# Optimization experiments

Hardware: AMD Instinct MI355X
Metric: run time of the kernel (lower is better)

The kernel has to match this reference:

```python
import jax, jax.numpy as jnp
import numpy as np

NH = 50000; NO = 50000; E = 500000; D = 256; L = 8; B = 512; C = 117


def setup_inputs() -> dict:
    key = jax.random.key(0)
    ks = jax.random.split(key, 32)
    s = 0.05
    inp = {
        'x_human': jax.random.normal(ks[0], (NH, D), jnp.float32),
        'x_object': jax.random.normal(ks[1], (NO, D), jnp.float32),
        'edge_index_ho': jax.random.randint(ks[2], (2, E), 0, NH),
        'edge_index_oh': jax.random.randint(ks[3], (2, E), 0, NO),
        'edge_attr_ho': jax.random.normal(ks[4], (E, 2), jnp.float32),
        'edge_attr_oh': jax.random.normal(ks[5], (E, 2), jnp.float32),
        'hbatch': jnp.sort(jax.random.randint(ks[6], (NH,), 0, B)),
        'obatch': jnp.sort(jax.random.randint(ks[7], (NO,), 0, B)),
    }
    # GATConv params per relation, stacked over L layers
    names = ['Wsrc', 'Wdst', 'asrc', 'adst', 'Wedge', 'aedge', 'bias']
    shapes = [(L, D, D), (L, D, D), (L, D), (L, D), (L, 2, D), (L, D), (L, D)]
    i = 8
    for rel in ['ho', 'oh']:
        for n, sh in zip(names, shapes):
            inp[f'{n}_{rel}'] = jax.random.normal(ks[i], sh, jnp.float32) * s
            i += 1
    inp['W_emlp'] = jax.random.normal(ks[i], (2, 32), jnp.float32) * s
    inp['b_emlp'] = jnp.zeros((32,), jnp.float32)
    inp['W_p1'] = jax.random.normal(ks[i + 1], (2 * D + 32, C), jnp.float32) * s
    inp['b_p1'] = jnp.zeros((C,), jnp.float32)
    inp['W_p2'] = jax.random.normal(ks[i + 2], (2 * D + 32, C), jnp.float32) * s
    inp['b_p2'] = jnp.zeros((C,), jnp.float32)
    return inp


def _gat(x_src, x_dst, ei, ea, Wsrc, Wdst, asrc, adst, Wedge, aedge, bias, num_dst):
    # PyG GATConv (heads=1, edge_dim=2, add_self_loops=False)
    h_src = x_src @ Wsrc                       # [Ns, D]
    h_dst = x_dst @ Wdst                       # [Nd, D]
    src, dst = ei[0], ei[1]
    a_s = h_src @ asrc                         # [Ns]
    a_d = h_dst @ adst                         # [Nd]
    a_e = (ea @ Wedge) @ aedge                 # [E]
    logit = jax.nn.leaky_relu(a_s[src] + a_d[dst] + a_e, 0.2)
    m = jax.ops.segment_max(logit, dst, num_segments=num_dst)
    ex = jnp.exp(logit - m[dst])
    denom = jax.ops.segment_sum(ex, dst, num_segments=num_dst)
    alpha = ex / denom[dst]                    # segment softmax over dst
    out = jax.ops.segment_sum(h_src[src] * alpha[:, None], dst, num_segments=num_dst)
    return out + bias


def _seg_mean(x, seg, num):
    s = jax.ops.segment_sum(x, seg, num_segments=num)
    cnt = jax.ops.segment_sum(jnp.ones((x.shape[0],), x.dtype), seg, num_segments=num)
    return s / jnp.maximum(cnt, 1.0)[:, None]


def reference(x_human, x_object, edge_index_ho, edge_index_oh, edge_attr_ho,
              edge_attr_oh, hbatch, obatch,
              Wsrc_ho, Wdst_ho, asrc_ho, adst_ho, Wedge_ho, aedge_ho, bias_ho,
              Wsrc_oh, Wdst_oh, asrc_oh, adst_oh, Wedge_oh, aedge_oh, bias_oh,
              W_emlp, b_emlp, W_p1, b_p1, W_p2, b_p2):
    xh, xo = x_human, x_object
    ph, po = None, None
    for l in range(L):
        nxo = _gat(xh, xo, edge_index_ho, edge_attr_ho, Wsrc_ho[l], Wdst_ho[l],
                   asrc_ho[l], adst_ho[l], Wedge_ho[l], aedge_ho[l], bias_ho[l], NO)
        nxh = _gat(xo, xh, edge_index_oh, edge_attr_oh, Wsrc_oh[l], Wdst_oh[l],
                   asrc_oh[l], adst_oh[l], Wedge_oh[l], aedge_oh[l], bias_oh[l], NH)
        nxh = jax.nn.relu(nxh)
        nxo = jax.nn.relu(nxo)
        if ph is not None:
            nxh = nxh + ph
            nxo = nxo + po
        ph, po = nxh, nxo
        xh, xo = nxh, nxo
    hpool = _seg_mean(xh, hbatch, B)           # [B, D]
    opool = _seg_mean(xo, obatch, B)           # [B, D]
    ea = jax.nn.relu(edge_attr_ho @ W_emlp + b_emlp)  # [E, 32]
    edge_batch = hbatch[edge_index_ho[0]]
    epool = _seg_mean(ea, edge_batch, B)       # [B, 32]
    graph_emb = jnp.concatenate([hpool, opool, epool], axis=-1)  # [B, 544]
    l1 = jax.nn.softmax(graph_emb @ W_p1 + b_p1, axis=1)
    l2 = jax.nn.softmax(graph_emb @ W_p2 + b_p2, axis=1)
    return jnp.stack((l1, l2), axis=1)         # [B, 2, C]
```

## Files before the change

### kernel.cpp

```cpp
#include <hip/hip_runtime.h>
#include <math.h>


#define NNODE 50000
#define EDG   500000
#define DIM   256
#define LAY   8
#define BB    512
#define CC    117
#define EMBD  544
#define SCB   49
#define HW    16384
#define HC    16
#define HNW   4

typedef short bf16x8 __attribute__((ext_vector_type(8)));
typedef float f32x4  __attribute__((ext_vector_type(4)));

static __device__ __forceinline__ float lrelu(float x){ return x >= 0.f ? x : 0.2f*x; }
static __device__ __forceinline__ unsigned short f2b(float f){
  unsigned int u = __float_as_uint(f);
  unsigned int r = (u + 0x7fffu + ((u >> 16) & 1u)) >> 16;
  return (unsigned short)r;
}
static __device__ __forceinline__ float b2f(unsigned short u){
  return __uint_as_float(((unsigned int)u) << 16);
}
static __device__ __forceinline__ float blo(unsigned int u){
  return __uint_as_float(u << 16);
}
static __device__ __forceinline__ float bhi(unsigned int u){
  return __uint_as_float(u & 0xffff0000u);
}
static __device__ __forceinline__ unsigned cvtpk(float lo, float hi){
  unsigned r;
  asm("v_cvt_pk_bf16_f32 %0, %1, %2" : "=v"(r) : "v"(lo), "v"(hi));
  return r;
}
static __device__ __forceinline__ float rdlane_f(float v, int id){
  return __uint_as_float(__builtin_amdgcn_readlane(__float_as_uint(v), id));
}
static __device__ __forceinline__ int rdlane_i(int v, int id){
  return __builtin_amdgcn_readlane(v, id);
}

static __device__ __forceinline__ void gload_lds16(const void* g, void* l){
  __builtin_amdgcn_global_load_lds((const __attribute__((address_space(1))) void*)g,
                                   (__attribute__((address_space(3))) void*)l,
                                   16, 0, 0);
}

__global__ void vcompute_k(const float* __restrict__ Wsho, const float* __restrict__ Wdho,
                           const float* __restrict__ asho, const float* __restrict__ adho,
                           const float* __restrict__ Wsoh, const float* __restrict__ Wdoh,
                           const float* __restrict__ asoh, const float* __restrict__ adoh,
                           float* __restrict__ vbuf){
  int gid = blockIdx.x*blockDim.x + threadIdx.x;
  int wv = gid >> 6, lane = gid & 63;
  if (wv >= 32*DIM) return;
  int p = wv >> 8, k = wv & 255;
  int which = p & 1, rel = (p>>1)&1, l = p>>2;
  const float* W; const float* a;
  if (rel==0){ W = which? Wdho : Wsho; a = which? adho : asho; }
  else       { W = which? Wdoh : Wsoh; a = which? adoh : asoh; }
  W += (size_t)l*DIM*DIM; a += (size_t)l*DIM;
  const float4* w4 = (const float4*)(W + (size_t)k*DIM);
  const float4* a4 = (const float4*)a;
  float4 wv4 = w4[lane], av4 = a4[lane];
  float s = wv4.x*av4.x + wv4.y*av4.y + wv4.z*av4.z + wv4.w*av4.w;
  for (int off=32; off; off>>=1) s += __shfl_xor(s, off);
  if (lane==0) vbuf[(size_t)p*DIM + k] = s;
}

__global__ void wecompute_k(const float* __restrict__ Weho, const float* __restrict__ aeho,
                            const float* __restrict__ Weoh, const float* __restrict__ aeoh,
                            float* __restrict__ webuf){
  int blk = blockIdx.x;
  int rel = blk & 1, l = blk >> 1;
  const float* We = rel? Weoh : Weho;
  const float* ae = rel? aeoh : aeho;
  int lane = threadIdx.x;
  const float4* w0 = (const float4*)(We + (size_t)l*2*DIM);
  const float4* w1 = (const float4*)(We + (size_t)l*2*DIM + DIM);
  const float4* a4 = (const float4*)(ae + (size_t)l*DIM);
  float4 av = a4[lane], x0 = w0[lane], x1 = w1[lane];
  float s0 = x0.x*av.x + x0.y*av.y + x0.z*av.z + x0.w*av.w;
  float s1 = x1.x*av.x + x1.y*av.y + x1.z*av.z + x1.w*av.w;
  for (int off=32; off; off>>=1){ s0 += __shfl_xor(s0, off); s1 += __shfl_xor(s1, off); }
  if (lane==0){ webuf[blk*2] = s0; webuf[blk*2+1] = s1; }
}

__global__ void histp_k(const int* __restrict__ ei_ho, const int* __restrict__ ei_oh,
                        int* __restrict__ phist){
  __shared__ int h[HW];
  int x = blockIdx.x, y = blockIdx.y, z = blockIdx.z, t = threadIdx.x;
  for (int i=t; i<HW; i+=256) h[i] = 0;
  __syncthreads();
  const int* keys = (z==0)? (ei_ho + EDG) : (z==1)? (ei_oh + EDG) : ei_ho;
  int lo = y << 14;
  int e0 = x * (EDG/HC), e1 = e0 + (EDG/HC);
  for (int e = e0 + t; e < e1; e += 256){
    int k = keys[e] - lo;
    if ((unsigned)k < (unsigned)HW) atomicAdd(&h[k], 1);
  }
  __syncthreads();
  int* dst = phist + (size_t)(((z*HNW + y)*HC + x))*HW;
  for (int i=t; i<HW; i+=256) dst[i] = h[i];
}

static __device__ __forceinline__ int4 phist_sum4(const int* __restrict__ phist,
                                                  int z, int idx){
  int win = idx >> 14, off = idx & (HW-1);
  const int* base = phist + (size_t)((z*HNW + win)*HC)*HW + off;
  int4 s = make_int4(0,0,0,0);
  #pragma unroll
  for (int c=0;c<HC;c++){
    int4 v = *(const int4*)(base + (size_t)c*HW);
    s.x += v.x; s.y += v.y; s.z += v.z; s.w += v.w;
  }
  return s;
}

__global__ void scanA_k(const int* __restrict__ phist, int* __restrict__ bsum){
  __shared__ int sh[256];
  int y = blockIdx.y, b = blockIdx.x, t = threadIdx.x;
  int idx = b*1024 + t*4;
  int s = 0;
  if (idx + 3 < NNODE){
    int4 v = phist_sum4(phist, y, idx);
    s = v.x + v.y + v.z + v.w;
  } else {
    for (int j=0;j<4;j++) if (idx+j < NNODE){
      int win = (idx+j) >> 14, off = (idx+j) & (HW-1);
      for (int c=0;c<HC;c++) s += phist[(size_t)((y*HNW+win)*HC+c)*HW + off];
    }
  }
  sh[t] = s; __syncthreads();
  for (int off=128; off; off>>=1){ if (t<off) sh[t] += sh[t+off]; __syncthreads(); }
  if (t==0) bsum[y*SCB + b] = sh[0];
}

__global__ void scanB_k(int* __restrict__ bsum, int* __restrict__ boff,
                        int* __restrict__ rp0, int* __restrict__ rp1, int* __restrict__ rp2){
  int t = threadIdx.x;
  if (t >= 3) return;
  int run = 0;
  for (int i=0;i<SCB;i++){ boff[t*SCB+i] = run; run += bsum[t*SCB+i]; }
  int* rp = (t==0)? rp0 : (t==1)? rp1 : rp2;
  rp[NNODE] = run;
}

__global__ void scanC_k(const int* __restrict__ phist, const int* __restrict__ boff,
                        int* __restrict__ rp0, int* __restrict__ rp1, int* __restrict__ rp2){
  __shared__ int sh[256];
  int y = blockIdx.y, b = blockIdx.x, t = threadIdx.x;
  int* rp = (y==0)? rp0 : (y==1)? rp1 : rp2;
  int idx = b*1024 + t*4;
  int c[4] = {0,0,0,0};
  if (idx + 3 < NNODE){
    int4 v = phist_sum4(phist, y, idx);
    c[0]=v.x; c[1]=v.y; c[2]=v.z; c[3]=v.w;
  } else {
    for (int j=0;j<4;j++) if (idx+j < NNODE){
      int win = (idx+j) >> 14, off = (idx+j) & (HW-1);
      for (int cc=0;cc<HC;cc++) c[j] += phist[(size_t)((y*HNW+win)*HC+cc)*HW + off];
    }
  }
  int mysum = c[0]+c[1]+c[2]+c[3];
  sh[t] = mysum; __syncthreads();
  for (int off=1; off<256; off<<=1){
    int v = (t>=off) ? sh[t-off] : 0;
    __syncthreads();
    sh[t] += v;
    __syncthreads();
  }
  int base = boff[y*SCB + b] + (sh[t] - mysum);
  int run = 0;
  for (int j=0;j<4;j++){
    if (idx+j < NNODE) rp[idx+j] = base + run;
    run += c[j];
  }
}

__global__ void scatter3_k(const int* __restrict__ ei_ho, const int* __restrict__ ei_oh,
                           const float* __restrict__ ea_ho, const float* __restrict__ ea_oh,
                           const int* __restrict__ rp0, const int* __restrict__ rp1,
                           const int* __restrict__ rp2, int* __restrict__ cur,
                           float4* __restrict__ rec0, float4* __restrict__ rec1,
                           float2* __restrict__ eap2){
  int e = blockIdx.x*blockDim.x + threadIdx.x;
  if (e >= EDG) return;
  int y = blockIdx.y;
  if (y == 0){
    int d = ei_ho[EDG + e];
    int pos = rp0[d] + atomicAdd(&cur[d], 1);
    rec0[pos] = make_float4(__int_as_float(ei_ho[e]), ea_ho[2*e], ea_ho[2*e+1], 0.f);
  } else if (y == 1){
    int d = ei_oh[EDG + e];
    int pos = rp1[d] + atomicAdd(&cur[NNODE + d], 1);
    rec1[pos] = make_float4(__int_as_float(ei_oh[e]), ea_oh[2*e], ea_oh[2*e+1], 0.f);
  } else {
    int s = ei_ho[e];
    int pos = rp2[s] + atomicAdd(&cur[2*NNODE + s], 1);
    eap2[pos] = make_float2(ea_ho[2*e], ea_ho[2*e+1]);
  }
}

__global__ void xcdg_k(const float* __restrict__ xh_in, const float* __restrict__ xo_in,
                       unsigned short* __restrict__ xhb, unsigned short* __restrict__ xob,
                       const float* __restrict__ vbuf, float* __restrict__ aset){
  int gid = blockIdx.x*blockDim.x + threadIdx.x;
  int w = gid >> 6, lane = gid & 63;
  if (w >= NNODE) return;
  int z = blockIdx.y;
  const float* X = z? xo_in : xh_in;
  unsigned short* O = z? xob : xhb;
  const float* v1 = vbuf + (size_t)(z? 2:0)*DIM;
  const float* v2 = vbuf + (size_t)(z? 1:3)*DIM;
  float* o1 = aset + (size_t)(z? 2:0)*NNODE;
  float* o2 = aset + (size_t)(z? 1:3)*NNODE;
  float4 xv = ((const float4*)(X + (size_t)w*DIM))[lane];
  uint2 ob; ob.x = cvtpk(xv.x, xv.y); ob.y = cvtpk(xv.z, xv.w);
  ((uint2*)O)[(size_t)w*64 + lane] = ob;
  float4 a = ((const float4*)v1)[lane];
  float4 b = ((const float4*)v2)[lane];
  float s1 = xv.x*a.x + xv.y*a.y + xv.z*a.z + xv.w*a.w;
  float s2 = xv.x*b.x + xv.y*b.y + xv.z*b.z + xv.w*b.w;
  for (int off=32; off; off>>=1){ s1 += __shfl_xor(s1, off); s2 += __shfl_xor(s2, off); }
  if (lane==0){ o1[w] = s1; o2[w] = s2; }
}

__global__ void wtconv_k(const float* __restrict__ Who, const float* __restrict__ Woh,
                         unsigned short* __restrict__ Wt){
  int gid = blockIdx.x*blockDim.x + threadIdx.x;
  int rel = gid >> 19;
  int rem = gid & ((1<<19)-1);
  int l = rem >> 16;
  int idx = rem & 65535;
  int n = idx >> 8, k = idx & 255;
  const float* W = rel ? Woh : Who;
  Wt[gid] = f2b(W[(size_t)l*65536 + (size_t)k*256 + n]);
}

__global__ __launch_bounds__(256) void gemmb2_k(const unsigned short* __restrict__ A0,
                                                const unsigned short* __restrict__ A1,
                                                const unsigned short* __restrict__ B0,
                                                const unsigned short* __restrict__ B1,
                                                unsigned short* __restrict__ H0,
                                                unsigned short* __restrict__ H1, int M){
  __shared__ __align__(16) unsigned short As[4096];
  __shared__ __align__(16) unsigned short Bs[4096];
  int z = blockIdx.z;
  const unsigned short* A  = z? A1 : A0;
  const unsigned short* Bt = z? B1 : B0;
  unsigned short* H        = z? H1 : H0;
  int tid = threadIdx.x;
  int col0 = blockIdx.x * 128;
  int row0 = blockIdx.y * 128;
  int w = tid >> 6, lane = tid & 63;
  int q = lane >> 4, ml = lane & 15;
  f32x4 acc[2][8];
  #pragma unroll
  for (int i=0;i<2;i++)
    #pragma unroll
    for (int j=0;j<8;j++) acc[i][j] = (f32x4){0.f,0.f,0.f,0.f};

  const unsigned short* srcA[2];
  const unsigned short* srcB[2];
  #pragma unroll
  for (int p=0;p<2;p++){
    int c = p*256 + w*64 + lane;
    int row = ((c>>6)<<4) | (c&15);
    int sq  = (c>>4)&3;
    int gr = row0 + row; if (gr >= M) gr = M-1;
    srcA[p] = A  + (size_t)gr*256 + sq*8;
    srcB[p] = Bt + (size_t)(col0 + row)*256 + sq*8;
  }

  for (int k0 = 0; k0 < 256; k0 += 32){
    #pragma unroll
    for (int p = 0; p < 2; ++p){
      gload_lds16(srcA[p], &As[(size_t)(p*256 + w*64)*8]);
      gload_lds16(srcB[p], &Bs[(size_t)(p*256 + w*64)*8]);
      srcA[p] += 32; srcB[p] += 32;
    }
    __syncthreads();
    bf16x8 a0 = *(const bf16x8*)&As[(((2*w+0)*4 + q)*16 + ml)*8];
    bf16x8 a1 = *(const bf16x8*)&As[(((2*w+1)*4 + q)*16 + ml)*8];
    #pragma unroll
    for (int nf = 0; nf < 8; ++nf){
      bf16x8 b = *(const bf16x8*)&Bs[((nf*4 + q)*16 + ml)*8];
      acc[0][nf] = __builtin_amdgcn_mfma_f32_16x16x32_bf16(a0, b, acc[0][nf], 0,0,0);
      acc[1][nf] = __builtin_amdgcn_mfma_f32_16x16x32_bf16(a1, b, acc[1][nf], 0,0,0);
    }
    __syncthreads();
  }
  #pragma unroll
  for (int mf = 0; mf < 2; ++mf){
    #pragma unroll
    for (int r = 0; r < 4; ++r){
      int gr = row0 + 32*w + 16*mf + q*4 + r;
      if (gr < M){
        #pragma unroll
        for (int nf = 0; nf < 8; ++nf)
          H[(size_t)gr*256 + col0 + nf*16 + ml] = f2b(acc[mf][nf][r]);
      }
    }
  }
}

__global__ void attn2_k(const int* __restrict__ rp0, const float4* __restrict__ rec0,
                        const int* __restrict__ rp1, const float4* __restrict__ rec1,
                        const float* __restrict__ cur_a, float* __restrict__ nxt_a,
                        const float* __restrict__ wepl,
                        const unsigned short* __restrict__ hs0,
                        const unsigned short* __restrict__ hs1,
                        const float* __restrict__ bias0, const float* __restrict__ bias1,
                        const unsigned short* __restrict__ xprev0,
                        const unsigned short* __restrict__ xprev1,
                        unsigned short* __restrict__ xnext0,
                        unsigned short* __restrict__ xnext1,
                        const float* __restrict__ vbl,
                        int hasRes, int doNext){
  int gid = blockIdx.x*blockDim.x + threadIdx.x;
  int w = gid >> 6, lane = gid & 63;
  if (w >= NNODE) return;
  int rel = blockIdx.y;
  const int* rowptr = rel? rp1 : rp0;
  const float4* rec = rel? rec1 : rec0;
  const float* a_s = cur_a + (size_t)(rel? 2:0)*NNODE;
  const float* a_d = cur_a + (size_t)(rel? 3:1)*NNODE;
  float w0 = wepl[rel? 2:0], w1 = wepl[rel? 3:1];
  const unsigned short* hs = rel? hs1 : hs0;
  const float* bias = rel? bias1 : bias0;
  const unsigned short* xprev = rel? xprev1 : xprev0;
  unsigned short* xnext = rel? xnext1 : xnext0;

  int st = rowptr[w], en = rowptr[w+1];
  int deg = en - st;
  float adv = a_d[w];

  float4 bv = ((const float4*)bias)[lane];
  uint2 rres = ((const uint2*)xprev)[(size_t)w*64 + lane];
  float4 va = ((const float4*)(vbl + (size_t)(rel? 0:2)*DIM))[lane];
  float4 vc = ((const float4*)(vbl + (size_t)(rel? 3:1)*DIM))[lane];

  float ax=0.f, ay=0.f, az=0.f, aw=0.f;
  if (deg > 0 && deg <= 64){
    int sreg = 0; float lg = -INFINITY;
    if (lane < deg){
      float4 r = rec[st + lane];
      sreg = __float_as_int(r.x);
      lg = lrelu(a_s[sreg] + adv + r.y*w0 + r.z*w1);
    }
    float mx = lg;
    for (int off=32; off; off>>=1) mx = fmaxf(mx, __shfl_xor(mx, off));
    float ex = (lane < deg) ? __expf(lg - mx) : 0.f;
    float sm = ex;
    for (int off=32; off; off>>=1) sm += __shfl_xor(sm, off);
    float wgt = ex * __builtin_amdgcn_rcpf(sm);
    int i = 0;
    for (; i + 7 < deg; i += 8){
      float wi[8]; const uint2* rp[8];
      #pragma unroll
      for (int j=0;j<8;j++){
        wi[j] = rdlane_f(wgt, i+j);
        rp[j] = (const uint2*)(hs + (size_t)rdlane_i(sreg, i+j)*DIM);
      }
      uint2 hv[8];
      #pragma unroll
      for (int j=0;j<8;j++) hv[j] = rp[j][lane];
      #pragma unroll
      for (int j=0;j<8;j++){
        ax += wi[j]*blo(hv[j].x); ay += wi[j]*bhi(hv[j].x);
        az += wi[j]*blo(hv[j].y); aw += wi[j]*bhi(hv[j].y);
      }
    }
    for (; i + 3 < deg; i += 4){
      float wi[4]; const uint2* rp[4];
      #pragma unroll
      for (int j=0;j<4;j++){
        wi[j] = rdlane_f(wgt, i+j);
        rp[j] = (const uint2*)(hs + (size_t)rdlane_i(sreg, i+j)*DIM);
      }
      uint2 hv[4];
      #pragma unroll
      for (int j=0;j<4;j++) hv[j] = rp[j][lane];
      #pragma unroll
      for (int j=0;j<4;j++){
        ax += wi[j]*blo(hv[j].x); ay += wi[j]*bhi(hv[j].x);
        az += wi[j]*blo(hv[j].y); aw += wi[j]*bhi(hv[j].y);
      }
    }
    for (; i < deg; ++i){
      float wi = rdlane_f(wgt, i);
      const uint2* rp = (const uint2*)(hs + (size_t)rdlane_i(sreg, i)*DIM);
      uint2 hv = rp[lane];
      ax += wi*blo(hv.x); ay += wi*bhi(hv.x);
      az += wi*blo(hv.y); aw += wi*bhi(hv.y);
    }
  } else if (deg > 64){
    const ushort4* h4 = (const ushort4*)hs;
    float mx = -INFINITY;
    for (int p = st + lane; p < en; p += 64){
      float4 r = rec[p];
      float lg = lrelu(a_s[__float_as_int(r.x)] + adv + r.y*w0 + r.z*w1);
      mx = fmaxf(mx, lg);
    }
    for (int off=32; off; off>>=1) mx = fmaxf(mx, __shfl_xor(mx, off));
    float sm = 0.f;
    for (int p = st + lane; p < en; p += 64){
      float4 r = rec[p];
      float lg = lrelu(a_s[__float_as_int(r.x)] + adv + r.y*w0 + r.z*w1);
      sm += __expf(lg - mx);
    }
    for (int off=32; off; off>>=1) sm += __shfl_xor(sm, off);
    float inv = __builtin_amdgcn_rcpf(sm);
    for (int p = st; p < en; ++p){
      float4 r = rec[p];
      int s = __float_as_int(r.x);
      float lg = lrelu(a_s[s] + adv + r.y*w0 + r.z*w1);
      float wgt = __expf(lg - mx) * inv;
      ushort4 hv = h4[(size_t)s*64 + lane];
      ax += wgt*b2f(hv.x); ay += wgt*b2f(hv.y); az += wgt*b2f(hv.z); aw += wgt*b2f(hv.w);
    }
  }

  float resw = hasRes ? 1.f : 0.f;
  float4 o;
  o.x = fmaxf(ax + bv.x, 0.f) + resw*blo(rres.x);
  o.y = fmaxf(ay + bv.y, 0.f) + resw*bhi(rres.x);
  o.z = fmaxf(az + bv.z, 0.f) + resw*blo(rres.y);
  o.w = fmaxf(aw + bv.w, 0.f) + resw*bhi(rres.y);
  uint2 ob; ob.x = cvtpk(o.x, o.y); ob.y = cvtpk(o.z, o.w);
  ((uint2*)xnext)[(size_t)w*64 + lane] = ob;
  if (doNext){
    float s1 = o.x*va.x + o.y*va.y + o.z*va.z + o.w*va.w;
    float s2 = o.x*vc.x + o.y*vc.y + o.z*vc.z + o.w*vc.w;
    for (int off=32; off; off>>=1){ s1 += __shfl_xor(s1, off); s2 += __shfl_xor(s2, off); }
    if (lane==0){
      float* asn = nxt_a + (size_t)(rel? 0:2)*NNODE;
      float* adn = nxt_a + (size_t)(rel? 3:1)*NNODE;
      asn[w] = s1; adn[w] = s2;
    }
  }
}

__device__ __forceinline__ int lowerb(const int* a, int n, int v){
  int lo=0, hi=n;
  while (lo < hi){ int m = (lo+hi)>>1; if (a[m] < v) lo = m+1; else hi = m; }
  return lo;
}

__global__ void pool2_k(const unsigned short* __restrict__ xh, const unsigned short* __restrict__ xo,
                        const int* __restrict__ hbatch, const int* __restrict__ obatch,
                        float* __restrict__ hpool, float* __restrict__ opool){
  int z = blockIdx.y;
  const unsigned short* x = z? xo : xh;
  const int* batch = z? obatch : hbatch;
  float* out = z? opool : hpool;
  int b = blockIdx.x, t = threadIdx.x;
  int st = lowerb(batch, NNODE, b), en = lowerb(batch, NNODE, b+1);
  float s = 0.f;
  for (int i=st;i<en;i++) s += b2f(x[(size_t)i*DIM + t]);
  out[(size_t)b*DIM + t] = s / fmaxf((float)(en - st), 1.f);
}

__global__ void epool_k(const int* __restrict__ rp_src, const int* __restrict__ hbatch,
                        const float2* __restrict__ eaperm, const float* __restrict__ Wem,
                        const float* __restrict__ bem, float* __restrict__ epool){
  __shared__ float ps[8][33];
  int b = blockIdx.x, t = threadIdx.x;
  int j = t & 31, g = t >> 5;
  int nst = lowerb(hbatch, NNODE, b), nen = lowerb(hbatch, NNODE, b+1);
  int est = rp_src[nst], een = rp_src[nen];
  float w0 = Wem[j], w1 = Wem[32+j], bb = bem[j];
  float s = 0.f;
  for (int p = est + g; p < een; p += 8){
    float2 e = eaperm[p];
    s += fmaxf(e.x*w0 + e.y*w1 + bb, 0.f);
  }
  ps[g][j] = s; __syncthreads();
  if (g == 0){
    float tot = 0.f;
    #pragma unroll
    for (int gg=0; gg<8; gg++) tot += ps[gg][j];
    epool[(size_t)b*32 + j] = tot / fmaxf((float)(een - est), 1.f);
  }
}

__global__ void head_k(const float* __restrict__ hpool, const float* __restrict__ opool,
                       const float* __restrict__ epool,
                       const float* __restrict__ Wp1, const float* __restrict__ bp1,
                       const float* __restrict__ Wp2, const float* __restrict__ bp2,
                       float* __restrict__ out){
  __shared__ float emb[EMBD];
  __shared__ float red[256];
  int b = blockIdx.x, t = threadIdx.x;
  emb[t] = hpool[(size_t)b*DIM + t];
  emb[DIM + t] = opool[(size_t)b*DIM + t];
  if (t < 32) emb[2*DIM + t] = epool[(size_t)b*32 + t];
  __syncthreads();
  for (int h = 0; h < 2; ++h){
    const float* Wp = h? Wp2 : Wp1;
    const float* bp = h? bp2 : bp1;
    float logit = -INFINITY;
    if (t < CC){
      float s = bp[t];
      for (int k=0;k<EMBD;k++) s += emb[k]*Wp[(size_t)k*CC + t];
      logit = s;
    }
    red[t] = logit; __syncthreads();
    for (int off=128; off; off>>=1){ if (t<off) red[t] = fmaxf(red[t], red[t+off]); __syncthreads(); }
    float mx = red[0]; __syncthreads();
    float ex = (t < CC) ? expf(logit - mx) : 0.f;
    red[t] = ex; __syncthreads();
    for (int off=128; off; off>>=1){ if (t<off) red[t] += red[t+off]; __syncthreads(); }
    float sm = red[0]; __syncthreads();
    if (t < CC) out[((size_t)b*2 + h)*CC + t] = ex / sm;
  }
}

extern "C" void kernel_launch(void* const* d_in, const int* in_sizes, int n_in,
                              void* d_out, int out_size, void* d_ws, size_t ws_size,
                              hipStream_t stream) {
  (void)in_sizes; (void)n_in; (void)out_size; (void)ws_size;
  const float* xh_in   = (const float*)d_in[0];
  const float* xo_in   = (const float*)d_in[1];
  const int*   ei_ho   = (const int*)d_in[2];
  const int*   ei_oh   = (const int*)d_in[3];
  const float* ea_ho   = (const float*)d_in[4];
  const float* ea_oh   = (const float*)d_in[5];
  const int*   hbatch  = (const int*)d_in[6];
  const int*   obatch  = (const int*)d_in[7];
  const float* Wsrc_ho = (const float*)d_in[8];
  const float* Wdst_ho = (const float*)d_in[9];
  const float* asrc_ho = (const float*)d_in[10];
  const float* adst_ho = (const float*)d_in[11];
  const float* Wedge_ho= (const float*)d_in[12];
  const float* aedge_ho= (const float*)d_in[13];
  const float* bias_ho = (const float*)d_in[14];
  const float* Wsrc_oh = (const float*)d_in[15];
  const float* Wdst_oh = (const float*)d_in[16];
  const float* asrc_oh = (const float*)d_in[17];
  const float* adst_oh = (const float*)d_in[18];
  const float* Wedge_oh= (const float*)d_in[19];
  const float* aedge_oh= (const float*)d_in[20];
  const float* bias_oh = (const float*)d_in[21];
  const float* W_emlp  = (const float*)d_in[22];
  const float* b_emlp  = (const float*)d_in[23];
  const float* W_p1    = (const float*)d_in[24];
  const float* b_p1    = (const float*)d_in[25];
  const float* W_p2    = (const float*)d_in[26];
  const float* b_p2    = (const float*)d_in[27];
  float* out = (float*)d_out;

  size_t ND = (size_t)NNODE*DIM;
  float* f = (float*)d_ws;
  float* aset0 = f;
  float* aset1 = aset0 + 4*NNODE;
  float* vbuf  = aset1 + 4*NNODE;
  float* webuf = vbuf + 32*DIM;
  float* hpool = webuf + 32;
  float* opool = hpool + (size_t)BB*DIM;
  float* epool = opool + (size_t)BB*DIM;
  float4* rec_ho  = (float4*)(epool + (size_t)BB*32);
  float4* rec_oh  = rec_ho + EDG;
  float2* eap_src = (float2*)(rec_oh + EDG);
  unsigned short* xhb0 = (unsigned short*)(eap_src + EDG);
  unsigned short* xhb1 = xhb0 + ND;
  unsigned short* xob0 = xhb1 + ND;
  unsigned short* xob1 = xob0 + ND;
  unsigned short* hSb0 = xob1 + ND;
  unsigned short* hSb1 = hSb0 + ND;
  unsigned short* Wtb  = hSb1 + ND;
  int* cur     = (int*)(Wtb + (size_t)2*LAY*DIM*DIM);
  int* rp_ho   = cur + 3*NNODE;
  int* rp_oh   = rp_ho + NNODE + 1;
  int* rp_src  = rp_oh + NNODE + 1;
  int* bsum    = rp_src + NNODE + 1;
  int* boff    = bsum + 3*SCB;
  int* phist   = boff + 3*SCB;

  hipMemsetAsync(cur, 0, sizeof(int)*3*NNODE, stream);
  vcompute_k<<<2048, 256, 0, stream>>>(Wsrc_ho, Wdst_ho, asrc_ho, adst_ho,
                                       Wsrc_oh, Wdst_oh, asrc_oh, adst_oh, vbuf);
  wecompute_k<<<16, 64, 0, stream>>>(Wedge_ho, aedge_ho, Wedge_oh, aedge_oh, webuf);
  wtconv_k<<<4096, 256, 0, stream>>>(Wsrc_ho, Wsrc_oh, Wtb);
  histp_k<<<dim3(HC, HNW, 3), 256, 0, stream>>>(ei_ho, ei_oh, phist);
  scanA_k<<<dim3(SCB, 3), 256, 0, stream>>>(phist, bsum);
  scanB_k<<<1, 64, 0, stream>>>(bsum, boff, rp_ho, rp_oh, rp_src);
  scanC_k<<<dim3(SCB, 3), 256, 0, stream>>>(phist, boff, rp_ho, rp_oh, rp_src);
  scatter3_k<<<dim3(1954, 3), 256, 0, stream>>>(ei_ho, ei_oh, ea_ho, ea_oh,
                                                rp_ho, rp_oh, rp_src, cur,
                                                rec_ho, rec_oh, eap_src);
  xcdg_k<<<dim3(12500, 2), 256, 0, stream>>>(xh_in, xo_in, xhb1, xob1, vbuf, aset0);

  const unsigned short* xh = xhb1;
  const unsigned short* xo = xob1;
  unsigned short* xh_bufs[2] = {xhb0, xhb1};
  unsigned short* xo_bufs[2] = {xob0, xob1};
  float* asets[2] = {aset0, aset1};
  for (int l = 0; l < LAY; ++l){
    unsigned short* xo_n = xo_bufs[l & 1];
    unsigned short* xh_n = xh_bufs[l & 1];
    float* cur_a = asets[l & 1];
    float* nxt_a = asets[(l & 1) ^ 1];
    int doNext = (l < LAY-1);
    int ln = doNext ? (l+1) : l;
    gemmb2_k<<<dim3(2, 391, 2), 256, 0, stream>>>(xh, xo,
                                                  Wtb + (size_t)l*DIM*DIM,
                                                  Wtb + (size_t)(LAY + l)*DIM*DIM,
                                                  hSb0, hSb1, NNODE);
    attn2_k<<<dim3(12500, 2), 256, 0, stream>>>(rp_ho, rec_ho,
                                                rp_oh, rec_oh,
                                                cur_a, nxt_a,
                                                webuf + (size_t)l*4,
                                                hSb0, hSb1,
                                                bias_ho + (size_t)l*DIM, bias_oh + (size_t)l*DIM,
                                                xo, xh, xo_n, xh_n,
                                                vbuf + (size_t)ln*4*DIM,
                                                l > 0, doNext);
    xh = xh_n; xo = xo_n;
  }

  pool2_k<<<dim3(BB, 2), 256, 0, stream>>>(xh, xo, hbatch, obatch, hpool, opool);
  epool_k<<<BB, 256, 0, stream>>>(rp_src, hbatch, eap_src, W_emlp, b_emlp, epool);
  head_k<<<BB, 256, 0, stream>>>(hpool, opool, epool, W_p1, b_p1, W_p2, b_p2, out);
}
```

Measured before the change: 1.451 ms.

## Split edge-softmax into separate per-edge logit kernel before aggregation

Adds an edge-parallel kernel that computes per-edge attention logits, stores them packed with source indices, and computes per-destination max and reciprocal sum using LDS staging. Storing the destination index in the previously unused record slot lets the logit pass run without per-node wave assignment. The attention kernel then only gathers logits and source indices and applies exp-normalize, which removes the wave reductions and the repeated logit recomputation on the high-degree path. In exchange it adds one kernel launch per layer, an extra write and read of an edge-sized buffer, and a serial per-thread segment loop for the max and sum. The new buffers alias the histogram scratch region.

Result: slower. 1.505 ms (+3.8%).

```diff
diff --git a/kernel.cpp b/kernel.cpp
--- a/kernel.cpp
+++ b/kernel.cpp
@@ -13,6 +13,7 @@
 #define HW    16384
 #define HC    16
 #define HNW   4
+#define LDSE  8192
 
 typedef short bf16x8 __attribute__((ext_vector_type(8)));
 typedef float f32x4  __attribute__((ext_vector_type(4)));
@@ -194,11 +195,13 @@
   if (y == 0){
     int d = ei_ho[EDG + e];
     int pos = rp0[d] + atomicAdd(&cur[d], 1);
-    rec0[pos] = make_float4(__int_as_float(ei_ho[e]), ea_ho[2*e], ea_ho[2*e+1], 0.f);
+    rec0[pos] = make_float4(__int_as_float(ei_ho[e]), ea_ho[2*e], ea_ho[2*e+1],
+                            __int_as_float(d));
   } else if (y == 1){
     int d = ei_oh[EDG + e];
     int pos = rp1[d] + atomicAdd(&cur[NNODE + d], 1);
-    rec1[pos] = make_float4(__int_as_float(ei_oh[e]), ea_oh[2*e], ea_oh[2*e+1], 0.f);
+    rec1[pos] = make_float4(__int_as_float(ei_oh[e]), ea_oh[2*e], ea_oh[2*e+1],
+                            __int_as_float(d));
   } else {
     int s = ei_ho[e];
     int pos = rp2[s] + atomicAdd(&cur[2*NNODE + s], 1);
@@ -309,10 +312,56 @@
   }
 }
 
-__global__ void attn2_k(const int* __restrict__ rp0, const float4* __restrict__ rec0,
-                        const int* __restrict__ rp1, const float4* __restrict__ rec1,
-                        const float* __restrict__ cur_a, float* __restrict__ nxt_a,
-                        const float* __restrict__ wepl,
+__global__ __launch_bounds__(256) void elsm_k(
+    const int* __restrict__ rp0, const float4* __restrict__ rec0,
+    const int* __restrict__ rp1, const float4* __restrict__ rec1,
+    const float* __restrict__ cur_a, const float* __restrict__ wepl,
+    uint2* __restrict__ lgsrc0, uint2* __restrict__ lgsrc1,
+    float2* __restrict__ ms0, float2* __restrict__ ms1){
+  __shared__ float lgs[LDSE];
+  int rel = blockIdx.y;
+  const int* rp = rel? rp1 : rp0;
+  const float4* rec = rel? rec1 : rec0;
+  const float* a_s = cur_a + (size_t)(rel? 2:0)*NNODE;
+  const float* a_d = cur_a + (size_t)(rel? 3:1)*NNODE;
+  float w0 = wepl[rel? 2:0], w1 = wepl[rel? 3:1];
+  uint2* lgsrc = rel? lgsrc1 : lgsrc0;
+  float2* ms = rel? ms1 : ms0;
+  int n0 = blockIdx.x * 128;
+  int n1 = n0 + 128; if (n1 > NNODE) n1 = NNODE;
+  int t = threadIdx.x;
+  int e0 = rp[n0], e1 = rp[n1];
+  bool fit = (e1 - e0) <= LDSE;
+  for (int e = e0 + t; e < e1; e += 256){
+    float4 r = rec[e];
+    int src = __float_as_int(r.x);
+    int dst = __float_as_int(r.w);
+    float lg = lrelu(a_s[src] + a_d[dst] + r.y*w0 + r.z*w1);
+    lgsrc[e] = make_uint2(__float_as_uint(lg), (unsigned)src);
+    if (fit) lgs[e - e0] = lg;
+  }
+  __syncthreads();
+  if (t < 128){
+    int n = n0 + t;
+    if (n < NNODE){
+      int st = rp[n], en = rp[n+1];
+      float m = -INFINITY, s = 0.f;
+      if (fit){
+        for (int p=st;p<en;p++) m = fmaxf(m, lgs[p-e0]);
+        for (int p=st;p<en;p++) s += __expf(lgs[p-e0] - m);
+      } else {
+        for (int p=st;p<en;p++) m = fmaxf(m, __uint_as_float(lgsrc[p].x));
+        for (int p=st;p<en;p++) s += __expf(__uint_as_float(lgsrc[p].x) - m);
+      }
+      ms[n] = make_float2(m, __builtin_amdgcn_rcpf(s));
+    }
+  }
+}
+
+__global__ void attn2_k(const int* __restrict__ rp0, const uint2* __restrict__ lgsrc0,
+                        const int* __restrict__ rp1, const uint2* __restrict__ lgsrc1,
+                        const float2* __restrict__ ms0, const float2* __restrict__ ms1,
+                        float* __restrict__ nxt_a,
                         const unsigned short* __restrict__ hs0,
                         const unsigned short* __restrict__ hs1,
                         const float* __restrict__ bias0, const float* __restrict__ bias1,
@@ -327,10 +376,8 @@
   if (w >= NNODE) return;
   int rel = blockIdx.y;
   const int* rowptr = rel? rp1 : rp0;
-  const float4* rec = rel? rec1 : rec0;
-  const float* a_s = cur_a + (size_t)(rel? 2:0)*NNODE;
-  const float* a_d = cur_a + (size_t)(rel? 3:1)*NNODE;
-  float w0 = wepl[rel? 2:0], w1 = wepl[rel? 3:1];
+  const uint2* lgsrc = rel? lgsrc1 : lgsrc0;
+  const float2* msb = rel? ms1 : ms0;
   const unsigned short* hs = rel? hs1 : hs0;
   const float* bias = rel? bias1 : bias0;
   const unsigned short* xprev = rel? xprev1 : xprev0;
@@ -338,7 +385,7 @@
 
   int st = rowptr[w], en = rowptr[w+1];
   int deg = en - st;
-  float adv = a_d[w];
+  float2 msv = msb[w];
 
   float4 bv = ((const float4*)bias)[lane];
   uint2 rres = ((const uint2*)xprev)[(size_t)w*64 + lane];
@@ -347,18 +394,12 @@
 
   float ax=0.f, ay=0.f, az=0.f, aw=0.f;
   if (deg > 0 && deg <= 64){
-    int sreg = 0; float lg = -INFINITY;
+    int sreg = 0; float wgt = 0.f;
     if (lane < deg){
-      float4 r = rec[st + lane];
-      sreg = __float_as_int(r.x);
-      lg = lrelu(a_s[sreg] + adv + r.y*w0 + r.z*w1);
-    }
-    float mx = lg;
-    for (int off=32; off; off>>=1) mx = fmaxf(mx, __shfl_xor(mx, off));
-    float ex = (lane < deg) ? __expf(lg - mx) : 0.f;
-    float sm = ex;
-    for (int off=32; off; off>>=1) sm += __shfl_xor(sm, off);
-    float wgt = ex * __builtin_amdgcn_rcpf(sm);
+      uint2 ls = lgsrc[st + lane];
+      sreg = (int)ls.y;
+      wgt = __expf(__uint_as_float(ls.x) - msv.x) * msv.y;
+    }
     int i = 0;
     for (; i + 7 < deg; i += 8){
       float wi[8]; const uint2* rp[8];
@@ -400,29 +441,13 @@
       az += wi*blo(hv.y); aw += wi*bhi(hv.y);
     }
   } else if (deg > 64){
-    const ushort4* h4 = (const ushort4*)hs;
-    float mx = -INFINITY;
-    for (int p = st + lane; p < en; p += 64){
-      float4 r = rec[p];
-      float lg = lrelu(a_s[__float_as_int(r.x)] + adv + r.y*w0 + r.z*w1);
-      mx = fmaxf(mx, lg);
-    }
-    for (int off=32; off; off>>=1) mx = fmaxf(mx, __shfl_xor(mx, off));
-    float sm = 0.f;
-    for (int p = st + lane; p < en; p += 64){
-      float4 r = rec[p];
-      float lg = lrelu(a_s[__float_as_int(r.x)] + adv + r.y*w0 + r.z*w1);
-      sm += __expf(lg - mx);
-    }
-    for (int off=32; off; off>>=1) sm += __shfl_xor(sm, off);
-    float inv = __builtin_amdgcn_rcpf(sm);
     for (int p = st; p < en; ++p){
-      float4 r = rec[p];
-      int s = __float_as_int(r.x);
-      float lg = lrelu(a_s[s] + adv + r.y*w0 + r.z*w1);
-      float wgt = __expf(lg - mx) * inv;
-      ushort4 hv = h4[(size_t)s*64 + lane];
-      ax += wgt*b2f(hv.x); ay += wgt*b2f(hv.y); az += wgt*b2f(hv.z); aw += wgt*b2f(hv.w);
+      uint2 ls = lgsrc[p];
+      float wgt = __expf(__uint_as_float(ls.x) - msv.x) * msv.y;
+      const uint2* rp = (const uint2*)(hs + (size_t)ls.y*DIM);
+      uint2 hv = rp[lane];
+      ax += wgt*blo(hv.x); ay += wgt*bhi(hv.x);
+      az += wgt*blo(hv.y); aw += wgt*bhi(hv.y);
     }
   }
 
@@ -581,6 +606,10 @@
   int* bsum    = rp_src + NNODE + 1;
   int* boff    = bsum + 3*SCB;
   int* phist   = boff + 3*SCB;
+  uint2*  lgsrc_ho = (uint2*)phist;
+  uint2*  lgsrc_oh = lgsrc_ho + EDG;
+  float2* msb_ho   = (float2*)(lgsrc_oh + EDG);
+  float2* msb_oh   = msb_ho + NNODE;
 
   hipMemsetAsync(cur, 0, sizeof(int)*3*NNODE, stream);
   vcompute_k<<<2048, 256, 0, stream>>>(Wsrc_ho, Wdst_ho, asrc_ho, adst_ho,
@@ -608,14 +637,17 @@
     float* nxt_a = asets[(l & 1) ^ 1];
     int doNext = (l < LAY-1);
     int ln = doNext ? (l+1) : l;
+    elsm_k<<<dim3(391, 2), 256, 0, stream>>>(rp_ho, rec_ho, rp_oh, rec_oh,
+                                             cur_a, webuf + (size_t)l*4,
+                                             lgsrc_ho, lgsrc_oh, msb_ho, msb_oh);
     gemmb2_k<<<dim3(2, 391, 2), 256, 0, stream>>>(xh, xo,
                                                   Wtb + (size_t)l*DIM*DIM,
                                                   Wtb + (size_t)(LAY + l)*DIM*DIM,
                                                   hSb0, hSb1, NNODE);
-    attn2_k<<<dim3(12500, 2), 256, 0, stream>>>(rp_ho, rec_ho,
-                                                rp_oh, rec_oh,
-                                                cur_a, nxt_a,
-                                                webuf + (size_t)l*4,
+    attn2_k<<<dim3(12500, 2), 256, 0, stream>>>(rp_ho, lgsrc_ho,
+                                                rp_oh, lgsrc_oh,
+                                                msb_ho, msb_oh,
+                                                nxt_a,
                                                 hSb0, hSb1,
                                                 bias_ho + (size_t)l*DIM, bias_oh + (size_t)l*DIM,
                                                 xo, xh, xo_n, xh_n,
```
